# Kernel tuning notes

Hardware: AMD Instinct MI355X
Metric: run time of the kernel (lower is better)

The kernel has to match this reference:

```python
import jax, jax.numpy as jnp
import numpy as np

B, N, DIM = 2, 2048, 2048
N_HEAD, N_KV_HEAD = 32, 8
HEAD_DIM = DIM // N_HEAD  # 64
NEG_INF = -1e9


def setup_inputs() -> dict:
    key = jax.random.key(0)
    ks = jax.random.split(key, 4)
    x = jax.random.normal(ks[0], (B, N, DIM), dtype=jnp.float32)
    Wq = jax.random.normal(ks[1], (DIM, N_HEAD * HEAD_DIM), dtype=jnp.float32) * (DIM ** -0.5)
    Wkv = jax.random.normal(ks[2], (DIM, 2 * N_KV_HEAD * HEAD_DIM), dtype=jnp.float32) * (DIM ** -0.5)
    Wo = jax.random.normal(ks[3], (N_HEAD * HEAD_DIM, DIM), dtype=jnp.float32) * (DIM ** -0.5)
    # RoPE angles: freqs = 1/theta^(2i/d), angle[p, i] = p * freqs[i]
    freqs = 1.0 / (10000.0 ** (jnp.arange(0, HEAD_DIM, 2, dtype=jnp.float32) / HEAD_DIM))
    angles = jnp.arange(N, dtype=jnp.float32)[:, None] * freqs[None, :]  # (N, HEAD_DIM//2)
    rope_cos = jnp.cos(angles)
    rope_sin = jnp.sin(angles)
    # additive causal mask (n, n)
    mask = jnp.where(jnp.tril(jnp.ones((N, N), dtype=bool)), 0.0, NEG_INF).astype(jnp.float32)
    return {"x": x, "Wq": Wq, "Wkv": Wkv, "Wo": Wo, "rope_cos": rope_cos, "rope_sin": rope_sin, "mask": mask, "start_pos": 0}


def apply_rope(x, cos, sin):
    # x: (b, n, h, d); cos/sin: (n, d//2). Complex mult on interleaved pairs.
    xr = x.reshape(*x.shape[:-1], HEAD_DIM // 2, 2)
    xe, xo = xr[..., 0], xr[..., 1]
    c = cos[None, :, None, :]
    s = sin[None, :, None, :]
    yr = xe * c - xo * s
    yi = xe * s + xo * c
    return jnp.stack([yr, yi], axis=-1).reshape(x.shape)


def reference(x, Wq, Wkv, Wo, rope_cos, rope_sin, mask, start_pos):
    b, n, _ = x.shape
    q = (x @ Wq).reshape(b, n, N_HEAD, HEAD_DIM)
    kv = (x @ Wkv).reshape(b, n, 2, N_KV_HEAD, HEAD_DIM)
    k, v = kv[:, :, 0], kv[:, :, 1]
    q = apply_rope(q, rope_cos, rope_sin)
    k = apply_rope(k, rope_cos, rope_sin)
    # repeat kv heads: 'b n h d -> b n (r h) d'
    r = N_HEAD // N_KV_HEAD
    k = jnp.tile(k, (1, 1, r, 1))
    v = jnp.tile(v, (1, 1, r, 1))
    scale = HEAD_DIM ** -0.5
    attn = jnp.einsum('bnhd,bmhd->bhnm', q, k) * scale + mask[None, None]
    attn = jax.nn.softmax(attn, axis=-1)
    out = jnp.einsum('bhnm,bmhd->bnhd', attn, v).reshape(b, n, N_HEAD * HEAD_DIM)
    return out @ Wo
```

## Files before the change

kernel.cpp:

```cpp
#include <hip/hip_runtime.h>


#define BSZ  2
#define NSEQ 2048
#define DIMD 2048
#define NH   32
#define NKV  8
#define HD   64

typedef __bf16 bf16x8 __attribute__((ext_vector_type(8)));
typedef __bf16 bf16x4 __attribute__((ext_vector_type(4)));
typedef __bf16 bf16x2 __attribute__((ext_vector_type(2)));
typedef float  floatx4 __attribute__((ext_vector_type(4)));

#define MFMA16(a, b, c) __builtin_amdgcn_mfma_f32_16x16x32_bf16(a, b, c, 0, 0, 0)

__device__ __forceinline__ void gload_lds16(const void* g, void* l) {
    __builtin_amdgcn_global_load_lds((const __attribute__((address_space(1))) void*)g,
                                     (__attribute__((address_space(3))) void*)l, 16, 0, 0);
}

__global__ void cvt_x_kernel(const float* __restrict__ in, __bf16* __restrict__ out, int n4) {
    int i = blockIdx.x * blockDim.x + threadIdx.x;
    if (i >= n4) return;
    float4 v = ((const float4*)in)[i];
    bf16x4 o;
    o[0] = (__bf16)v.x; o[1] = (__bf16)v.y; o[2] = (__bf16)v.z; o[3] = (__bf16)v.w;
    ((bf16x4*)out)[i] = o;
}

__global__ void transpose_cvt_kernel(const float* __restrict__ W, __bf16* __restrict__ Wt,
                                     int C, int K) {
    __shared__ float t[32][33];
    int c0 = blockIdx.x * 32, r0 = blockIdx.y * 32;
    int lx = threadIdx.x & 31, ly = threadIdx.x >> 5;
    for (int i = 0; i < 32; i += 8)
        t[ly + i][lx] = W[(size_t)(r0 + ly + i) * C + c0 + lx];
    __syncthreads();
    for (int i = 0; i < 32; i += 8)
        Wt[(size_t)(c0 + ly + i) * K + r0 + lx] = (__bf16)t[lx][ly + i];
}

__global__ __launch_bounds__(256) void gemm_qkv_kernel(
    const __bf16* __restrict__ A, const __bf16* __restrict__ Bt,
    const float* __restrict__ cosb, const float* __restrict__ sinb,
    __bf16* __restrict__ Qo, __bf16* __restrict__ Ko, __bf16* __restrict__ Vo) {
    __shared__ __align__(16) __bf16 As[128 * 64];
    __shared__ __align__(16) __bf16 Bs[128 * 64];
    __shared__ bf16x2 trig[128 * 33];

    int tid = threadIdx.x;
    int wave = tid >> 6, lane = tid & 63;
    int wr = wave >> 1, wc = wave & 1;
    int quad = lane >> 4, l16 = lane & 15;
    int t0 = blockIdx.y * 128;
    int p0 = blockIdx.x * 128;
    bool isV = (p0 >= 2560);

    if (!isV) {
        const float* cb = cosb + (size_t)(t0 & 2047) * 32;
        const float* sb = sinb + (size_t)(t0 & 2047) * 32;
        for (int i4 = tid; i4 < 1024; i4 += 256) {
            int idx = i4 * 4, row = idx >> 5, col = idx & 31;
            float4 cv = *(const float4*)(cb + idx);
            float4 sv4 = *(const float4*)(sb + idx);
            bf16x2* d = &trig[row * 33 + col];
            bf16x2 e0, e1, e2, e3;
            e0[0] = (__bf16)cv.x; e0[1] = (__bf16)sv4.x;
            e1[0] = (__bf16)cv.y; e1[1] = (__bf16)sv4.y;
            e2[0] = (__bf16)cv.z; e2[1] = (__bf16)sv4.z;
            e3[0] = (__bf16)cv.w; e3[1] = (__bf16)sv4.w;
            d[0] = e0; d[1] = e1; d[2] = e2; d[3] = e3;
        }
    }

    floatx4 acc[4][4] = {};
    const __bf16* Abase = A + (size_t)t0 * DIMD;
    const __bf16* Bbase = Bt + (size_t)p0 * DIMD;
    int sw8 = (l16 & 7) << 3;

    for (int k0 = 0; k0 < DIMD; k0 += 64) {
        __syncthreads();
        for (int r = 0; r < 4; ++r) {
            int obase = r * 2048 + wave * 512;
            int o = obase + lane * 8;
            int row = o >> 6;
            int el = (o & 63) ^ ((row & 7) << 3);
            gload_lds16(Abase + (size_t)row * DIMD + k0 + el, &As[obase]);
            gload_lds16(Bbase + (size_t)row * DIMD + k0 + el, &Bs[obase]);
        }
        __syncthreads();
        for (int c = 0; c < 2; ++c) {
            int ko = (c * 32 + quad * 8) ^ sw8;
            bf16x8 tf[4], pf[4];
            for (int j = 0; j < 4; ++j)
                tf[j] = *(const bf16x8*)&As[(wr * 64 + j * 16 + l16) * 64 + ko];
            for (int i = 0; i < 4; ++i)
                pf[i] = *(const bf16x8*)&Bs[(wc * 64 + i * 16 + l16) * 64 + ko];
            for (int i = 0; i < 4; ++i)
                for (int j = 0; j < 4; ++j)
                    acc[i][j] = MFMA16(pf[i], tf[j], acc[i][j]);
        }
    }

    for (int j = 0; j < 4; ++j) {
        int nl = wr * 64 + j * 16 + l16;
        int t = t0 + nl;
        int b = t >> 11, n = t & 2047;
        for (int i = 0; i < 4; ++i) {
            float x0 = acc[i][j][0], x1 = acc[i][j][1];
            float x2 = acc[i][j][2], x3 = acc[i][j][3];
            int dq = i * 16 + quad * 4;
            if (!isV) {
                int d2 = dq >> 1;
                bf16x2 cs0 = trig[nl * 33 + d2];
                bf16x2 cs1 = trig[nl * 33 + d2 + 1];
                float c0 = (float)cs0[0], s0 = (float)cs0[1];
                float c1 = (float)cs1[0], s1 = (float)cs1[1];
                bf16x4 o;
                o[0] = (__bf16)(x0 * c0 - x1 * s0);
                o[1] = (__bf16)(x0 * s0 + x1 * c0);
                o[2] = (__bf16)(x2 * c1 - x3 * s1);
                o[3] = (__bf16)(x2 * s1 + x3 * c1);
                if (p0 < 2048) {
                    int h = (p0 >> 6) + wc;
                    *(bf16x4*)&Qo[((size_t)(b * NH + h) * NSEQ + n) * HD + dq] = o;
                } else {
                    int kvh = ((p0 - 2048) >> 6) + wc;
                    *(bf16x4*)&Ko[((size_t)(b * NKV + kvh) * NSEQ + n) * HD + dq] = o;
                }
            } else {
                int kvh = ((p0 - 2560) >> 6) + wc;
                size_t base = ((size_t)(b * NKV + kvh)) * HD;
                Vo[(base + dq + 0) * NSEQ + n] = (__bf16)x0;
                Vo[(base + dq + 1) * NSEQ + n] = (__bf16)x1;
                Vo[(base + dq + 2) * NSEQ + n] = (__bf16)x2;
                Vo[(base + dq + 3) * NSEQ + n] = (__bf16)x3;
            }
        }
    }
}

__global__ __launch_bounds__(256) void gemm_bt_db_kernel(
    const __bf16* __restrict__ A, const __bf16* __restrict__ Bt,
    float* __restrict__ C, int M, int N, int K) {
    __shared__ __align__(16) __bf16 As[2][128 * 64];
    __shared__ __align__(16) __bf16 Bs[2][128 * 64];
    int tid = threadIdx.x;
    int wave = tid >> 6, lane = tid & 63;
    int wr = wave >> 1, wc = wave & 1;
    int quad = lane >> 4, l16 = lane & 15;
    int m0 = blockIdx.y * 128, n0 = blockIdx.x * 128;

    floatx4 acc[4][4] = {};
    const __bf16* Abase = A + (size_t)m0 * K;
    const __bf16* Bbase = Bt + (size_t)n0 * K;
    int sw8 = (l16 & 7) << 3;

    auto stage = [&](int k0, int bi) {
        for (int r = 0; r < 4; ++r) {
            int obase = r * 2048 + wave * 512;
            int o = obase + lane * 8;
            int row = o >> 6;
            int el = (o & 63) ^ ((row & 7) << 3);
            gload_lds16(Abase + (size_t)row * K + k0 + el, &As[bi][obase]);
            gload_lds16(Bbase + (size_t)row * K + k0 + el, &Bs[bi][obase]);
        }
    };

    stage(0, 0);
    int pb = 0;
    for (int k0 = 0; k0 < K; k0 += 64) {
        __syncthreads();
        if (k0 + 64 < K) stage(k0 + 64, pb ^ 1);
        for (int c = 0; c < 2; ++c) {
            int ko = (c * 32 + quad * 8) ^ sw8;
            bf16x8 af[4], bfr[4];
            for (int i = 0; i < 4; ++i)
                af[i] = *(const bf16x8*)&As[pb][(wr * 64 + i * 16 + l16) * 64 + ko];
            for (int j = 0; j < 4; ++j)
                bfr[j] = *(const bf16x8*)&Bs[pb][(wc * 64 + j * 16 + l16) * 64 + ko];
            for (int i = 0; i < 4; ++i)
                for (int j = 0; j < 4; ++j)
                    acc[i][j] = MFMA16(af[i], bfr[j], acc[i][j]);
        }
        pb ^= 1;
    }
    for (int i = 0; i < 4; ++i) {
        int row = m0 + wr * 64 + i * 16 + quad * 4;
        for (int j = 0; j < 4; ++j) {
            int col = n0 + wc * 64 + j * 16 + l16;
            float* Cp = C + (size_t)row * N + col;
            for (int r = 0; r < 4; ++r)
                Cp[(size_t)r * N] = acc[i][j][r];
        }
    }
}

__global__ __launch_bounds__(256) void attn_kernel(
    const __bf16* __restrict__ Q, const __bf16* __restrict__ K,
    const __bf16* __restrict__ Vt, __bf16* __restrict__ O) {
    __shared__ __align__(16) __bf16 Kl[2][64 * 64];
    __shared__ __align__(16) __bf16 Vl[2][64 * 64];
    __shared__ __align__(16) __bf16 Pl[4][16 * 72];

    int tid = threadIdx.x;
    int wave = tid >> 6, lane = tid & 63;
    int quad = lane >> 4, l16 = lane & 15;
    int bk = blockIdx.x;
    int b = bk >> 3, kvh = bk & 7;
    int h = kvh + wave * 8;

    const __bf16* Qbase = Q + ((size_t)(b * NH + h)) * NSEQ * HD;
    const __bf16* Kbase = K + ((size_t)(b * NKV + kvh)) * NSEQ * HD;
    const __bf16* Vbase = Vt + ((size_t)(b * NKV + kvh)) * HD * NSEQ;
    __bf16* P = &Pl[wave][0];
    const float c2 = 0.125f * 1.44269504f;
    int swk = (l16 & 7) << 3;

    auto stage = [&](int kt, int bi) {
        for (int r = 0; r < 2; ++r) {
            int obase = r * 2048 + wave * 512;
            int o = obase + lane * 8;
            int row = o >> 6;
            int el = (o & 63) ^ ((row & 7) << 3);
            gload_lds16(Kbase + (size_t)kt * 4096 + row * 64 + el, &Kl[bi][obase]);
            gload_lds16(Vbase + (size_t)row * NSEQ + kt * 64 + el, &Vl[bi][obase]);
        }
    };

    int pb = 0;
    stage(0, 0);

    for (int half = 0; half < 2; ++half) {
        int qt = half ? blockIdx.y : 63 - blockIdx.y;
        int q0 = qt * 32;

        bf16x8 qf[2][2];
        for (int s = 0; s < 2; ++s) {
            int qrow = q0 + s * 16 + l16;
            qf[s][0] = *(const bf16x8*)(Qbase + (size_t)qrow * HD + quad * 8);
            qf[s][1] = *(const bf16x8*)(Qbase + (size_t)qrow * HD + 32 + quad * 8);
        }

        floatx4 oa[2][4] = {};
        float l_[2] = {0.0f, 0.0f};
        int ktmax = (q0 + 31) >> 6;

        for (int kt = 0; kt <= ktmax; ++kt) {
            __syncthreads();
            if (kt < ktmax) stage(kt + 1, pb ^ 1);
            else if (half == 0) stage(0, pb ^ 1);

            bf16x8 kf[4][2], vf[4][2];
            for (int j = 0; j < 4; ++j) {
                int rr = (j * 16 + l16) * 64;
                kf[j][0] = *(const bf16x8*)&Kl[pb][rr + ((quad * 8) ^ swk)];
                kf[j][1] = *(const bf16x8*)&Kl[pb][rr + ((quad * 8 + 32) ^ swk)];
                vf[j][0] = *(const bf16x8*)&Vl[pb][rr + ((quad * 8) ^ swk)];
                vf[j][1] = *(const bf16x8*)&Vl[pb][rr + ((quad * 8 + 32) ^ swk)];
            }

            bool diag = (kt == ktmax);
            for (int s = 0; s < 2; ++s) {
                int q_l = q0 + s * 16 + l16;
                for (int j = 0; j < 4; ++j) {
                    floatx4 sv = {0.f, 0.f, 0.f, 0.f};
                    sv = MFMA16(kf[j][0], qf[s][0], sv);
                    sv = MFMA16(kf[j][1], qf[s][1], sv);
                    bf16x4 pk;
                    if (diag) {
                        int kvb = kt * 64 + j * 16 + quad * 4;
                        for (int r = 0; r < 4; ++r) {
                            float p = __builtin_exp2f(sv[r] * c2);
                            if (kvb + r > q_l) p = 0.0f;
                            l_[s] += p;
                            pk[r] = (__bf16)p;
                        }
                    } else {
                        for (int r = 0; r < 4; ++r) {
                            float p = __builtin_exp2f(sv[r] * c2);
                            l_[s] += p;
                            pk[r] = (__bf16)p;
                        }
                    }
                    *(bf16x4*)&P[l16 * 72 + j * 16 + quad * 4] = pk;
                }
                bf16x8 pb0 = *(const bf16x8*)&P[l16 * 72 + quad * 8];
                bf16x8 pb1 = *(const bf16x8*)&P[l16 * 72 + 32 + quad * 8];
                for (int j = 0; j < 4; ++j) {
                    oa[s][j] = MFMA16(vf[j][0], pb0, oa[s][j]);
                    oa[s][j] = MFMA16(vf[j][1], pb1, oa[s][j]);
                }
            }
            pb ^= 1;
        }

        for (int s = 0; s < 2; ++s) {
            float lf = l_[s];
            lf += __shfl_xor(lf, 16, 64);
            lf += __shfl_xor(lf, 32, 64);
            float inv = 1.0f / lf;
            int n = q0 + s * 16 + l16;
            __bf16* Op = O + ((size_t)(b * NSEQ + n)) * (NH * HD) + h * HD + quad * 4;
            for (int j = 0; j < 4; ++j) {
                bf16x4 ov;
                for (int r = 0; r < 4; ++r) ov[r] = (__bf16)(oa[s][j][r] * inv);
                *(bf16x4*)(Op + j * 16) = ov;
            }
        }
    }
}

extern "C" void kernel_launch(void* const* d_in, const int* in_sizes, int n_in,
                              void* d_out, int out_size, void* d_ws, size_t ws_size,
                              hipStream_t stream) {
    const float* x   = (const float*)d_in[0];
    const float* Wq  = (const float*)d_in[1];
    const float* Wkv = (const float*)d_in[2];
    const float* Wo  = (const float*)d_in[3];
    const float* rc  = (const float*)d_in[4];
    const float* rs  = (const float*)d_in[5];
    float* out = (float*)d_out;
    char* ws = (char*)d_ws;

    __bf16* xb    = (__bf16*)(ws + 0);
    __bf16* wqkvt = (__bf16*)(ws + 16777216);
    __bf16* wot   = (__bf16*)(ws + 29360128);
    __bf16* Qb    = (__bf16*)(ws + 37748736);
    __bf16* Kb    = (__bf16*)(ws + 54525952);
    __bf16* Vtb   = (__bf16*)(ws + 58720256);
    __bf16* attnb = (__bf16*)(ws + 62914560);

    cvt_x_kernel<<<8192, 256, 0, stream>>>(x, xb, 2097152);
    transpose_cvt_kernel<<<dim3(64, 64), 256, 0, stream>>>(Wq, wqkvt, 2048, 2048);
    transpose_cvt_kernel<<<dim3(32, 64), 256, 0, stream>>>(Wkv, wqkvt + (size_t)2048 * 2048, 1024, 2048);
    transpose_cvt_kernel<<<dim3(64, 64), 256, 0, stream>>>(Wo, wot, 2048, 2048);

    gemm_qkv_kernel<<<dim3(24, 32), 256, 0, stream>>>(xb, wqkvt, rc, rs, Qb, Kb, Vtb);

    attn_kernel<<<dim3(16, 32), 256, 0, stream>>>(Qb, Kb, Vtb, attnb);

    gemm_bt_db_kernel<<<dim3(16, 32), 256, 0, stream>>>(attnb, wot, out, 4096, 2048, 2048);
}
```

Baseline: 328.2 us.

## Use shared 256x256 four-stage pipelined GEMM core for QKV and output projections

Both projection GEMMs now run on a common 256x256-tile, 512-thread core. It uses a 4-deep LDS ring filled by global_load_lds, explicit vmcnt waits with barriers that do not drain outstanding loads, an XOR swizzle, and raised wave priority around the MFMA block. The aim is to hide global load latency and get more reuse from each staged tile. RoPE cos/sin are now read straight from global memory in the epilogue instead of being staged in LDS. The trade-off is fewer blocks: 192 and 128, on a chip with many CUs. That can leave CUs idle, and the larger tiles raise register pressure.

```diff
diff --git a/kernel.cpp b/kernel.cpp
--- a/kernel.cpp
+++ b/kernel.cpp
@@ -14,6 +14,16 @@
 typedef float  floatx4 __attribute__((ext_vector_type(4)));
 
 #define MFMA16(a, b, c) __builtin_amdgcn_mfma_f32_16x16x32_bf16(a, b, c, 0, 0, 0)
+
+#define WAITV(n) asm volatile("s_waitcnt vmcnt(" #n ")" ::: "memory")
+
+__device__ __forceinline__ void barrier_nodrain() {
+    asm volatile("" ::: "memory");
+    __builtin_amdgcn_sched_barrier(0);
+    __builtin_amdgcn_s_barrier();
+    __builtin_amdgcn_sched_barrier(0);
+    asm volatile("" ::: "memory");
+}
 
 __device__ __forceinline__ void gload_lds16(const void* g, void* l) {
     __builtin_amdgcn_global_load_lds((const __attribute__((address_space(1))) void*)g,
@@ -41,97 +51,119 @@
         Wt[(size_t)(c0 + ly + i) * K + r0 + lx] = (__bf16)t[lx][ly + i];
 }
 
-__global__ __launch_bounds__(256) void gemm_qkv_kernel(
+
+__device__ __forceinline__ void stage256(const __bf16* __restrict__ Ab,
+                                         const __bf16* __restrict__ Bb,
+                                         __bf16* As, __bf16* Bs,
+                                         int s, int kt, int wave, int lane) {
+    #pragma unroll
+    for (int r = 0; r < 2; ++r) {
+        int o = r * 4096 + wave * 512 + lane * 8;
+        int row = o >> 5;
+        int chunk = (o >> 3) & 3;
+        int el = (chunk ^ ((row & 3) ^ ((row >> 2) & 3))) << 3;
+        __bf16* dA = As + s * 8192 + r * 4096 + wave * 512;
+        __bf16* dB = Bs + s * 8192 + r * 4096 + wave * 512;
+        gload_lds16(Ab + (size_t)row * DIMD + kt * 32 + el, dA);
+        gload_lds16(Bb + (size_t)row * DIMD + kt * 32 + el, dB);
+    }
+}
+
+__device__ __forceinline__ void compute256(const __bf16* As, const __bf16* Bs, int s,
+                                           int wm, int wn, int quad, int l16,
+                                           floatx4 (&acc)[8][4]) {
+    int kq = (quad ^ ((l16 & 3) ^ ((l16 >> 2) & 3))) << 3;
+    const __bf16* Ab = As + s * 8192;
+    const __bf16* Bb = Bs + s * 8192;
+    bf16x8 af[8], bf[4];
+    #pragma unroll
+    for (int i = 0; i < 8; ++i)
+        af[i] = *(const bf16x8*)&Ab[(wm * 128 + i * 16 + l16) * 32 + kq];
+    #pragma unroll
+    for (int j = 0; j < 4; ++j)
+        bf[j] = *(const bf16x8*)&Bb[(wn * 64 + j * 16 + l16) * 32 + kq];
+    __builtin_amdgcn_s_setprio(1);
+    #pragma unroll
+    for (int i = 0; i < 8; ++i)
+        #pragma unroll
+        for (int j = 0; j < 4; ++j)
+            acc[i][j] = MFMA16(af[i], bf[j], acc[i][j]);
+    __builtin_amdgcn_s_setprio(0);
+}
+
+__device__ __forceinline__ void gemm256_core(const __bf16* __restrict__ Ab,
+                                             const __bf16* __restrict__ Bb,
+                                             __bf16* As, __bf16* Bs,
+                                             floatx4 (&acc)[8][4]) {
+    int tid = threadIdx.x;
+    int wave = tid >> 6, lane = tid & 63;
+    int wm = wave >> 2, wn = wave & 3;
+    int quad = lane >> 4, l16 = lane & 15;
+
+    stage256(Ab, Bb, As, Bs, 0, 0, wave, lane);
+    stage256(Ab, Bb, As, Bs, 1, 1, wave, lane);
+    stage256(Ab, Bb, As, Bs, 2, 2, wave, lane);
+
+    #pragma unroll 4
+    for (int ks = 0; ks < 61; ++ks) {
+        WAITV(8);
+        barrier_nodrain();
+        stage256(Ab, Bb, As, Bs, (ks + 3) & 3, ks + 3, wave, lane);
+        compute256(As, Bs, ks & 3, wm, wn, quad, l16, acc);
+    }
+    WAITV(8); barrier_nodrain(); compute256(As, Bs, 1, wm, wn, quad, l16, acc);
+    WAITV(4); barrier_nodrain(); compute256(As, Bs, 2, wm, wn, quad, l16, acc);
+    WAITV(0); barrier_nodrain(); compute256(As, Bs, 3, wm, wn, quad, l16, acc);
+}
+
+__global__ __launch_bounds__(512, 2) void gemm_qkv_kernel(
     const __bf16* __restrict__ A, const __bf16* __restrict__ Bt,
     const float* __restrict__ cosb, const float* __restrict__ sinb,
     __bf16* __restrict__ Qo, __bf16* __restrict__ Ko, __bf16* __restrict__ Vo) {
-    __shared__ __align__(16) __bf16 As[128 * 64];
-    __shared__ __align__(16) __bf16 Bs[128 * 64];
-    __shared__ bf16x2 trig[128 * 33];
+    __shared__ __align__(16) __bf16 As[4 * 8192];
+    __shared__ __align__(16) __bf16 Bs[4 * 8192];
+    int p0 = blockIdx.x * 256;
+    int t0 = blockIdx.y * 256;
+
+    floatx4 acc[8][4] = {};
+    gemm256_core(Bt + (size_t)p0 * DIMD, A + (size_t)t0 * DIMD, As, Bs, acc);
 
     int tid = threadIdx.x;
     int wave = tid >> 6, lane = tid & 63;
-    int wr = wave >> 1, wc = wave & 1;
+    int wm = wave >> 2, wn = wave & 3;
     int quad = lane >> 4, l16 = lane & 15;
-    int t0 = blockIdx.y * 128;
-    int p0 = blockIdx.x * 128;
-    bool isV = (p0 >= 2560);
-
-    if (!isV) {
-        const float* cb = cosb + (size_t)(t0 & 2047) * 32;
-        const float* sb = sinb + (size_t)(t0 & 2047) * 32;
-        for (int i4 = tid; i4 < 1024; i4 += 256) {
-            int idx = i4 * 4, row = idx >> 5, col = idx & 31;
-            float4 cv = *(const float4*)(cb + idx);
-            float4 sv4 = *(const float4*)(sb + idx);
-            bf16x2* d = &trig[row * 33 + col];
-            bf16x2 e0, e1, e2, e3;
-            e0[0] = (__bf16)cv.x; e0[1] = (__bf16)sv4.x;
-            e1[0] = (__bf16)cv.y; e1[1] = (__bf16)sv4.y;
-            e2[0] = (__bf16)cv.z; e2[1] = (__bf16)sv4.z;
-            e3[0] = (__bf16)cv.w; e3[1] = (__bf16)sv4.w;
-            d[0] = e0; d[1] = e1; d[2] = e2; d[3] = e3;
-        }
-    }
-
-    floatx4 acc[4][4] = {};
-    const __bf16* Abase = A + (size_t)t0 * DIMD;
-    const __bf16* Bbase = Bt + (size_t)p0 * DIMD;
-    int sw8 = (l16 & 7) << 3;
-
-    for (int k0 = 0; k0 < DIMD; k0 += 64) {
-        __syncthreads();
-        for (int r = 0; r < 4; ++r) {
-            int obase = r * 2048 + wave * 512;
-            int o = obase + lane * 8;
-            int row = o >> 6;
-            int el = (o & 63) ^ ((row & 7) << 3);
-            gload_lds16(Abase + (size_t)row * DIMD + k0 + el, &As[obase]);
-            gload_lds16(Bbase + (size_t)row * DIMD + k0 + el, &Bs[obase]);
-        }
-        __syncthreads();
-        for (int c = 0; c < 2; ++c) {
-            int ko = (c * 32 + quad * 8) ^ sw8;
-            bf16x8 tf[4], pf[4];
-            for (int j = 0; j < 4; ++j)
-                tf[j] = *(const bf16x8*)&As[(wr * 64 + j * 16 + l16) * 64 + ko];
-            for (int i = 0; i < 4; ++i)
-                pf[i] = *(const bf16x8*)&Bs[(wc * 64 + i * 16 + l16) * 64 + ko];
-            for (int i = 0; i < 4; ++i)
-                for (int j = 0; j < 4; ++j)
-                    acc[i][j] = MFMA16(pf[i], tf[j], acc[i][j]);
-        }
-    }
-
-    for (int j = 0; j < 4; ++j) {
-        int nl = wr * 64 + j * 16 + l16;
-        int t = t0 + nl;
-        int b = t >> 11, n = t & 2047;
-        for (int i = 0; i < 4; ++i) {
+    bool isQ = p0 < 2048;
+    bool isV = p0 >= 2560;
+
+    #pragma unroll
+    for (int i = 0; i < 8; ++i) {
+        int pp = p0 + wm * 128 + i * 16 + quad * 4;
+        int dq = pp & 63;
+        #pragma unroll
+        for (int j = 0; j < 4; ++j) {
+            int t = t0 + wn * 64 + j * 16 + l16;
+            int b = t >> 11, n = t & 2047;
             float x0 = acc[i][j][0], x1 = acc[i][j][1];
             float x2 = acc[i][j][2], x3 = acc[i][j][3];
-            int dq = i * 16 + quad * 4;
             if (!isV) {
                 int d2 = dq >> 1;
-                bf16x2 cs0 = trig[nl * 33 + d2];
-                bf16x2 cs1 = trig[nl * 33 + d2 + 1];
-                float c0 = (float)cs0[0], s0 = (float)cs0[1];
-                float c1 = (float)cs1[0], s1 = (float)cs1[1];
+                float2 cv = *(const float2*)(cosb + (size_t)n * 32 + d2);
+                float2 sv = *(const float2*)(sinb + (size_t)n * 32 + d2);
                 bf16x4 o;
-                o[0] = (__bf16)(x0 * c0 - x1 * s0);
-                o[1] = (__bf16)(x0 * s0 + x1 * c0);
-                o[2] = (__bf16)(x2 * c1 - x3 * s1);
-                o[3] = (__bf16)(x2 * s1 + x3 * c1);
-                if (p0 < 2048) {
-                    int h = (p0 >> 6) + wc;
+                o[0] = (__bf16)(x0 * cv.x - x1 * sv.x);
+                o[1] = (__bf16)(x0 * sv.x + x1 * cv.x);
+                o[2] = (__bf16)(x2 * cv.y - x3 * sv.y);
+                o[3] = (__bf16)(x2 * sv.y + x3 * cv.y);
+                if (isQ) {
+                    int h = pp >> 6;
                     *(bf16x4*)&Qo[((size_t)(b * NH + h) * NSEQ + n) * HD + dq] = o;
                 } else {
-                    int kvh = ((p0 - 2048) >> 6) + wc;
+                    int kvh = (pp - 2048) >> 6;
                     *(bf16x4*)&Ko[((size_t)(b * NKV + kvh) * NSEQ + n) * HD + dq] = o;
                 }
             } else {
-                int kvh = ((p0 - 2560) >> 6) + wc;
-                size_t base = ((size_t)(b * NKV + kvh)) * HD;
+                int kvh = (pp - 2560) >> 6;
+                size_t base = (size_t)(b * NKV + kvh) * HD;
                 Vo[(base + dq + 0) * NSEQ + n] = (__bf16)x0;
                 Vo[(base + dq + 1) * NSEQ + n] = (__bf16)x1;
                 Vo[(base + dq + 2) * NSEQ + n] = (__bf16)x2;
@@ -141,58 +173,32 @@
     }
 }
 
-__global__ __launch_bounds__(256) void gemm_bt_db_kernel(
+__global__ __launch_bounds__(512, 2) void gemm_out_kernel(
     const __bf16* __restrict__ A, const __bf16* __restrict__ Bt,
-    float* __restrict__ C, int M, int N, int K) {
-    __shared__ __align__(16) __bf16 As[2][128 * 64];
-    __shared__ __align__(16) __bf16 Bs[2][128 * 64];
+    float* __restrict__ C) {
+    __shared__ __align__(16) __bf16 As[4 * 8192];
+    __shared__ __align__(16) __bf16 Bs[4 * 8192];
+    int n0 = blockIdx.x * 256;
+    int m0 = blockIdx.y * 256;
+
+    floatx4 acc[8][4] = {};
+    gemm256_core(A + (size_t)m0 * DIMD, Bt + (size_t)n0 * DIMD, As, Bs, acc);
+
     int tid = threadIdx.x;
     int wave = tid >> 6, lane = tid & 63;
-    int wr = wave >> 1, wc = wave & 1;
+    int wm = wave >> 2, wn = wave & 3;
     int quad = lane >> 4, l16 = lane & 15;
-    int m0 = blockIdx.y * 128, n0 = blockIdx.x * 128;
-
-    floatx4 acc[4][4] = {};
-    const __bf16* Abase = A + (size_t)m0 * K;
-    const __bf16* Bbase = Bt + (size_t)n0 * K;
-    int sw8 = (l16 & 7) << 3;
-
-    auto stage = [&](int k0, int bi) {
-        for (int r = 0; r < 4; ++r) {
-            int obase = r * 2048 + wave * 512;
-            int o = obase + lane * 8;
-            int row = o >> 6;
-            int el = (o & 63) ^ ((row & 7) << 3);
-            gload_lds16(Abase + (size_t)row * K + k0 + el, &As[bi][obase]);
-            gload_lds16(Bbase + (size_t)row * K + k0 + el, &Bs[bi][obase]);
-        }
-    };
-
-    stage(0, 0);
-    int pb = 0;
-    for (int k0 = 0; k0 < K; k0 += 64) {
-        __syncthreads();
-        if (k0 + 64 < K) stage(k0 + 64, pb ^ 1);
-        for (int c = 0; c < 2; ++c) {
-            int ko = (c * 32 + quad * 8) ^ sw8;
-            bf16x8 af[4], bfr[4];
-            for (int i = 0; i < 4; ++i)
-                af[i] = *(const bf16x8*)&As[pb][(wr * 64 + i * 16 + l16) * 64 + ko];
-            for (int j = 0; j < 4; ++j)
-                bfr[j] = *(const bf16x8*)&Bs[pb][(wc * 64 + j * 16 + l16) * 64 + ko];
-            for (int i = 0; i < 4; ++i)
-                for (int j = 0; j < 4; ++j)
-                    acc[i][j] = MFMA16(af[i], bfr[j], acc[i][j]);
-        }
-        pb ^= 1;
-    }
-    for (int i = 0; i < 4; ++i) {
-        int row = m0 + wr * 64 + i * 16 + quad * 4;
+    #pragma unroll
+    for (int i = 0; i < 8; ++i) {
+        int row = m0 + wm * 128 + i * 16 + quad * 4;
+        #pragma unroll
         for (int j = 0; j < 4; ++j) {
-            int col = n0 + wc * 64 + j * 16 + l16;
-            float* Cp = C + (size_t)row * N + col;
-            for (int r = 0; r < 4; ++r)
-                Cp[(size_t)r * N] = acc[i][j][r];
+            int col = n0 + wn * 64 + j * 16 + l16;
+            float* Cp = C + (size_t)row * 2048 + col;
+            Cp[0]    = acc[i][j][0];
+            Cp[2048] = acc[i][j][1];
+            Cp[4096] = acc[i][j][2];
+            Cp[6144] = acc[i][j][3];
         }
     }
 }
@@ -337,9 +343,9 @@
     transpose_cvt_kernel<<<dim3(32, 64), 256, 0, stream>>>(Wkv, wqkvt + (size_t)2048 * 2048, 1024, 2048);
     transpose_cvt_kernel<<<dim3(64, 64), 256, 0, stream>>>(Wo, wot, 2048, 2048);
 
-    gemm_qkv_kernel<<<dim3(24, 32), 256, 0, stream>>>(xb, wqkvt, rc, rs, Qb, Kb, Vtb);
+    gemm_qkv_kernel<<<dim3(12, 16), 512, 0, stream>>>(xb, wqkvt, rc, rs, Qb, Kb, Vtb);
 
     attn_kernel<<<dim3(16, 32), 256, 0, stream>>>(Qb, Kb, Vtb, attnb);
 
-    gemm_bt_db_kernel<<<dim3(16, 32), 256, 0, stream>>>(attnb, wot, out, 4096, 2048, 2048);
-}
+    gemm_out_kernel<<<dim3(8, 16), 512, 0, stream>>>(attnb, wot, out);
+}
```

Result: slower. 351.9 us (+7.2%).
